# Performance work log

Hardware: AMD Instinct MI355X
Metric: run time of the kernel (lower is better)

The kernel has to match this reference:

```python
import jax, jax.numpy as jnp
import numpy as np

IN_F, OUT_F, GROUP = 4096, 4096, 128
N_GROUPS = IN_F // GROUP
NIB_SHIFTS = jnp.arange(8, dtype=jnp.int32) * 4  # 8 nibbles per int32


def dequantize(qweight, qzeros, scales, g_idx):
    """GPTQ/exllama 4-bit grouped dequant -> fp16 weight [K, N]."""
    # unpack qweight: [K//8, N] int32 -> [K//8, 8, N] nibbles -> [K, N]
    w_q = (qweight[:, None, :] >> NIB_SHIFTS[None, :, None]) & 0xF
    w_q = w_q.reshape(-1, qweight.shape[1])  # [K, N]
    # unpack qzeros: [G, N//8] int32 -> [G, N//8, 8] -> [G, N]
    z_q = (qzeros[:, :, None] >> NIB_SHIFTS[None, None, :]) & 0xF
    z_q = z_q.reshape(qzeros.shape[0], -1)  # [G, N]
    # exllama stores zero-points minus one: w = (q - (z + 1)) * scale
    z_rows = z_q[g_idx]            # [K, N] int32
    s_rows = scales[g_idx]         # [K, N] fp16
    return (w_q - z_rows - 1).astype(jnp.float16) * s_rows


def setup_inputs() -> dict:
    key = jax.random.key(0)
    k_x, k_qw, k_qz, k_s, k_b = jax.random.split(key, 5)
    x = jax.random.normal(k_x, (4, 2048, IN_F), dtype=jnp.float16)
    qweight = jax.random.randint(k_qw, (IN_F // 8, OUT_F), 0, 2147483647, dtype=jnp.int32)
    qzeros = jax.random.randint(k_qz, (N_GROUPS, OUT_F // 8), 0, 2147483647, dtype=jnp.int32)
    scales = (jax.random.uniform(k_s, (N_GROUPS, OUT_F), dtype=jnp.float32) * 0.01 + 0.001).astype(jnp.float16)
    g_idx = (jnp.arange(IN_F, dtype=jnp.int32) // GROUP).astype(jnp.int32)
    bias = (jax.random.normal(k_b, (OUT_F,), dtype=jnp.float32) * 0.02).astype(jnp.float16)
    return {"x": x, "qweight": qweight, "qzeros": qzeros, "scales": scales, "g_idx": g_idx, "bias": bias}


def reference(x, qweight, qzeros, scales, g_idx, bias):
    W = dequantize(qweight, qzeros, scales, g_idx)      # [K, N] fp16
    lead = x.shape[:-1]
    out = jnp.dot(x.reshape(-1, x.shape[-1]), W)        # fp16 GEMM, [T, N]
    out = out + bias
    return out.reshape(lead + (W.shape[1],))
```

## Files before the change

### kernel.cpp

```cpp
#include <hip/hip_runtime.h>
#include <hip/hip_bf16.h>
#include <stdint.h>

#define M_TOT 8192
#define N_TOT 4096
#define K_TOT 4096
#define GROUP 128


using f32x4  = __attribute__((ext_vector_type(4))) float;
using bf16x8 = __attribute__((ext_vector_type(8))) __bf16;

typedef __attribute__((address_space(3))) void as3_void;
typedef const __attribute__((address_space(1))) void as1_void;

__global__ __launch_bounds__(256) void cast_x(const float* __restrict__ x,
                                              __bf16* __restrict__ xb) {
    const size_t t = (size_t)blockIdx.x * 256 + threadIdx.x;
    const float4 f0 = *(const float4*)(x + t * 8);
    const float4 f1 = *(const float4*)(x + t * 8 + 4);
    bf16x8 v;
    v[0]=(__bf16)f0.x; v[1]=(__bf16)f0.y; v[2]=(__bf16)f0.z; v[3]=(__bf16)f0.w;
    v[4]=(__bf16)f1.x; v[5]=(__bf16)f1.y; v[6]=(__bf16)f1.z; v[7]=(__bf16)f1.w;
    *(bf16x8*)(xb + t * 8) = v;
}

__global__ __launch_bounds__(256) void dequant_w(
    const int*   __restrict__ qweight,
    const int*   __restrict__ qzeros,
    const float* __restrict__ scales,
    const int*   __restrict__ g_idx,
    __bf16* __restrict__ Wt)
{
    __shared__ __align__(16) unsigned short T[64 * 72];
    const int k0  = blockIdx.x * 64;
    const int n0  = blockIdx.y * 64;
    const int g   = g_idx[k0];
    const int tid = threadIdx.x;

    #pragma unroll
    for (int i = 0; i < 2; ++i) {
        const int idx = tid + i * 256;
        const int r   = idx >> 6;
        const int n   = idx & 63;
        const int qi  = qweight[(size_t)((k0 >> 3) + r) * N_TOT + n0 + n];
        const int zi  = qzeros[g * (N_TOT / 8) + ((n0 + n) >> 3)];
        const float s = scales[g * N_TOT + n0 + n];
        const float zs = (float)(((zi >> ((n & 7) * 4)) & 0xF) + 1) * s;
        bf16x8 v;
        #pragma unroll
        for (int j = 0; j < 8; ++j)
            v[j] = (__bf16)((float)((qi >> (4 * j)) & 0xF) * s - zs);
        *(bf16x8*)&T[n * 72 + r * 8] = v;
    }
    __syncthreads();

    const int n = tid >> 2;
    const int c = (tid & 3) * 16;
    const bf16x8 a = *(const bf16x8*)&T[n * 72 + c];
    const bf16x8 b = *(const bf16x8*)&T[n * 72 + c + 8];
    __bf16* dst = Wt + (size_t)(n0 + n) * K_TOT + k0 + c;
    *(bf16x8*)dst = a;
    *(bf16x8*)(dst + 8) = b;
}

#define GBM 256
#define GBN 256
#define GBK 64
#define NKT (K_TOT / GBK)

#define BAR() do { asm volatile("" ::: "memory"); \
                   __builtin_amdgcn_s_barrier();  \
                   asm volatile("" ::: "memory"); } while (0)
#define WAIT_LGKM0() asm volatile("s_waitcnt lgkmcnt(0)" ::: "memory")
#define WAIT_VM4()   asm volatile("s_waitcnt vmcnt(4)"   ::: "memory")
#define WAIT_VM0()   asm volatile("s_waitcnt vmcnt(0)"   ::: "memory")

#define GPHASE(q, STAGE_STMT)                                                 \
    {                                                                         \
        bf16x8 av[2][2];                                                      \
        _Pragma("unroll")                                                     \
        for (int ks = 0; ks < 2; ++ks) {                                      \
            av[0][ks] = ldA(buf, 2 * (q), ks);                                \
            av[1][ks] = ldA(buf, 2 * (q) + 1, ks);                            \
        }                                                                     \
        STAGE_STMT;                                                           \
        BAR();                                                                \
        WAIT_LGKM0();                                                         \
        __builtin_amdgcn_s_setprio(1);                                        \
        _Pragma("unroll")                                                     \
        for (int ks = 0; ks < 2; ++ks)                                        \
            _Pragma("unroll")                                                 \
            for (int mtl = 0; mtl < 2; ++mtl)                                 \
                _Pragma("unroll")                                             \
                for (int nt = 0; nt < 4; ++nt)                                \
                    acc[2 * (q) + mtl][nt] =                                  \
                        __builtin_amdgcn_mfma_f32_16x16x32_bf16(              \
                            av[mtl][ks], bv[nt][ks], acc[2 * (q) + mtl][nt],  \
                            0, 0, 0);                                         \
        __builtin_amdgcn_s_setprio(0);                                        \
        BAR();                                                                \
    }

__global__ __launch_bounds__(512, 2) void gemm8p(
    const __bf16* __restrict__ xb,
    const __bf16* __restrict__ Wt,
    const float*  __restrict__ bias,
    float* __restrict__ out)
{
    __shared__ __align__(16) unsigned short LDS[2][2][GBM * GBK];

    const int tid  = threadIdx.x;
    const int wid  = tid >> 6;
    const int lane = tid & 63;
    const int l15  = lane & 15;
    const int quad = lane >> 4;

    int bid = blockIdx.x;
    bid = (bid & 7) * (512 >> 3) + (bid >> 3);
    const int tn = bid & (N_TOT / GBN - 1);
    const int tm = bid >> 4;
    const int m0 = tm * GBM;
    const int n0 = tn * GBN;

    const int wm = (wid >> 2) * 128;
    const int wn = (wid & 3) * 64;

    f32x4 acc[8][4];
    #pragma unroll
    for (int i = 0; i < 8; ++i)
        #pragma unroll
        for (int j = 0; j < 4; ++j)
            acc[i][j] = (f32x4)0.f;

    auto stage = [&](int bf, int mat, int h, const __bf16* __restrict__ base,
                     int row0, int kt) {
        #pragma unroll
        for (int j = 0; j < 2; ++j) {
            const int c  = j * 512 + tid;
            const int rl = c >> 3;
            const int kc = (c & 7) ^ (rl & 7);
            const __bf16* ga = base + (size_t)(row0 + h * 128 + rl) * K_TOT
                             + kt * GBK + kc * 8;
            __builtin_amdgcn_global_load_lds((as1_void*)ga,
                (as3_void*)&LDS[bf][mat][h * 8192 + (j * 512 + wid * 64) * 8],
                16, 0, 0);
        }
    };
    auto ldA = [&](int bf, int mt, int ks) -> bf16x8 {
        const int r = wm + mt * 16 + l15;
        return *(const bf16x8*)
            &LDS[bf][0][r * GBK + (((ks * 4 + quad) ^ (r & 7)) << 3)];
    };
    auto ldB = [&](int bf, int nt, int ks) -> bf16x8 {
        const int r = wn + nt * 16 + l15;
        return *(const bf16x8*)
            &LDS[bf][1][r * GBK + (((ks * 4 + quad) ^ (r & 7)) << 3)];
    };

    stage(0, 0, 0, xb, m0, 0); stage(0, 0, 1, xb, m0, 0);
    stage(0, 1, 0, Wt, n0, 0); stage(0, 1, 1, Wt, n0, 0);
    stage(1, 1, 0, Wt, n0, 1); stage(1, 1, 1, Wt, n0, 1);
    WAIT_VM4();
    BAR();

    bf16x8 bv[4][2];

    for (int t = 0; t < NKT; ++t) {
        const int buf = t & 1;

        {
            #pragma unroll
            for (int nt = 0; nt < 4; ++nt)
                #pragma unroll
                for (int ks = 0; ks < 2; ++ks)
                    bv[nt][ks] = ldB(buf, nt, ks);
            bf16x8 av[2][2];
            #pragma unroll
            for (int ks = 0; ks < 2; ++ks) {
                av[0][ks] = ldA(buf, 0, ks);
                av[1][ks] = ldA(buf, 1, ks);
            }
            if (t + 1 < NKT) stage(buf ^ 1, 0, 0, xb, m0, t + 1);
            BAR();
            WAIT_LGKM0();
            __builtin_amdgcn_s_setprio(1);
            #pragma unroll
            for (int ks = 0; ks < 2; ++ks)
                #pragma unroll
                for (int mtl = 0; mtl < 2; ++mtl)
                    #pragma unroll
                    for (int nt = 0; nt < 4; ++nt)
                        acc[mtl][nt] = __builtin_amdgcn_mfma_f32_16x16x32_bf16(
                            av[mtl][ks], bv[nt][ks], acc[mtl][nt], 0, 0, 0);
            __builtin_amdgcn_s_setprio(0);
            BAR();
        }
        GPHASE(1, if (t + 1 < NKT) stage(buf ^ 1, 0, 1, xb, m0, t + 1));
        GPHASE(2, if (t + 2 < NKT) stage(buf, 1, 0, Wt, n0, t + 2));
        GPHASE(3, if (t + 2 < NKT) stage(buf, 1, 1, Wt, n0, t + 2));

        if (t < NKT - 2) { WAIT_VM4(); } else { WAIT_VM0(); }
    }

    #pragma unroll
    for (int nt = 0; nt < 4; ++nt) {
        const int col = n0 + wn + nt * 16 + l15;
        const float bb = bias[col];
        #pragma unroll
        for (int mt = 0; mt < 8; ++mt) {
            const int rowb = m0 + wm + mt * 16 + quad * 4;
            #pragma unroll
            for (int i = 0; i < 4; ++i)
                out[(size_t)(rowb + i) * N_TOT + col] = acc[mt][nt][i] + bb;
        }
    }
}

#define FBM 256
#define FBN 128
#define FBKP 72

__global__ __launch_bounds__(256, 2) void gptq_gemm_fused(
    const float* __restrict__ x, const int* __restrict__ qweight,
    const int* __restrict__ qzeros, const float* __restrict__ scales,
    const int* __restrict__ g_idx, const float* __restrict__ bias,
    float* __restrict__ out)
{
    __shared__ __align__(16) unsigned short As[FBM * FBKP];
    __shared__ __align__(16) unsigned short Bt[FBN * FBKP];

    const int tid  = threadIdx.x;
    const int wave = tid >> 6;
    const int lane = tid & 63;
    const int n0 = blockIdx.x * FBN;
    const int m0 = blockIdx.y * FBM;
    const int wm = (wave >> 1) * 64;
    const int wn = (wave & 1) * 64;
    const int l15  = lane & 15;
    const int quad = lane >> 4;

    f32x4 acc[2][4][4];
    #pragma unroll
    for (int mi = 0; mi < 2; ++mi)
        #pragma unroll
        for (int i = 0; i < 4; ++i)
            #pragma unroll
            for (int j = 0; j < 4; ++j)
                acc[mi][i][j] = (f32x4)0.f;

    const int nb  = tid & 31;
    const int r   = tid >> 5;
    const int zsh = (nb & 7) * 4;

    for (int kt = 0; kt < K_TOT / 64; ++kt) {
        const int k0 = kt * 64;
        #pragma unroll
        for (int i = 0; i < 8; ++i) {
            const int c   = tid + i * 256;
            const int row = c >> 3;
            const int cb  = (c & 7) << 3;
            const float* xp = x + (size_t)(m0 + row) * K_TOT + (k0 + cb);
            const float4 f0 = *(const float4*)xp;
            const float4 f1 = *(const float4*)(xp + 4);
            bf16x8 v;
            v[0]=(__bf16)f0.x; v[1]=(__bf16)f0.y; v[2]=(__bf16)f0.z; v[3]=(__bf16)f0.w;
            v[4]=(__bf16)f1.x; v[5]=(__bf16)f1.y; v[6]=(__bf16)f1.z; v[7]=(__bf16)f1.w;
            *(bf16x8*)&As[row * FBKP + cb] = v;
        }
        const int g    = g_idx[k0];
        const int qrow = (k0 >> 3) + r;
        #pragma unroll
        for (int dn = 0; dn < 4; ++dn) {
            const int n  = nb + dn * 32;
            const int qi = qweight[(size_t)qrow * N_TOT + (n0 + n)];
            const int zi = qzeros[g * (N_TOT / 8) + ((n0 + n) >> 3)];
            const float s = scales[g * N_TOT + (n0 + n)];
            const float zs = (float)(((zi >> zsh) & 0xF) + 1) * s;
            bf16x8 v;
            #pragma unroll
            for (int j = 0; j < 8; ++j)
                v[j] = (__bf16)((float)((qi >> (4 * j)) & 0xF) * s - zs);
            *(bf16x8*)&Bt[n * FBKP + r * 8] = v;
        }
        __syncthreads();
        #pragma unroll
        for (int ks = 0; ks < 2; ++ks) {
            bf16x8 bvv[4];
            #pragma unroll
            for (int nt = 0; nt < 4; ++nt)
                bvv[nt] = *(const bf16x8*)&Bt[(wn + nt * 16 + l15) * FBKP + ks * 32 + quad * 8];
            #pragma unroll
            for (int mi = 0; mi < 2; ++mi) {
                bf16x8 av[4];
                #pragma unroll
                for (int mt = 0; mt < 4; ++mt)
                    av[mt] = *(const bf16x8*)&As[(mi * 128 + wm + mt * 16 + l15) * FBKP + ks * 32 + quad * 8];
                #pragma unroll
                for (int mt = 0; mt < 4; ++mt)
                    #pragma unroll
                    for (int nt = 0; nt < 4; ++nt)
                        acc[mi][mt][nt] = __builtin_amdgcn_mfma_f32_16x16x32_bf16(
                            av[mt], bvv[nt], acc[mi][mt][nt], 0, 0, 0);
            }
        }
        __syncthreads();
    }
    #pragma unroll
    for (int mi = 0; mi < 2; ++mi)
        #pragma unroll
        for (int nt = 0; nt < 4; ++nt) {
            const int col = n0 + wn + nt * 16 + l15;
            const float bvv = bias[col];
            #pragma unroll
            for (int mt = 0; mt < 4; ++mt) {
                const int rowb = m0 + mi * 128 + wm + mt * 16 + quad * 4;
                #pragma unroll
                for (int i = 0; i < 4; ++i)
                    out[(size_t)(rowb + i) * N_TOT + col] = acc[mi][mt][nt][i] + bvv;
            }
        }
}

extern "C" void kernel_launch(void* const* d_in, const int* in_sizes, int n_in,
                              void* d_out, int out_size, void* d_ws, size_t ws_size,
                              hipStream_t stream) {
    const float* x  = (const float*)d_in[0];
    const int*   qw = (const int*)d_in[1];
    const int*   qz = (const int*)d_in[2];
    const float* sc = (const float*)d_in[3];
    const int*   gi = (const int*)d_in[4];
    const float* bs = (const float*)d_in[5];
    float* out = (float*)d_out;

    const size_t xb_bytes = (size_t)M_TOT * K_TOT * 2;
    const size_t wt_bytes = (size_t)N_TOT * K_TOT * 2;

    if (ws_size >= xb_bytes + wt_bytes) {
        __bf16* xb = (__bf16*)d_ws;
        __bf16* Wt = (__bf16*)((char*)d_ws + xb_bytes);
        cast_x<<<dim3((M_TOT * K_TOT) / (256 * 8)), dim3(256), 0, stream>>>(x, xb);
        dequant_w<<<dim3(K_TOT / 64, N_TOT / 64), dim3(256), 0, stream>>>(qw, qz, sc, gi, Wt);
        gemm8p<<<dim3((M_TOT / GBM) * (N_TOT / GBN)), dim3(512), 0, stream>>>(xb, Wt, bs, out);
    } else {
        gptq_gemm_fused<<<dim3(N_TOT / FBN, M_TOT / FBM), dim3(256), 0, stream>>>(
            x, qw, qz, sc, gi, bs, out);
    }
}
```

Before: 456.2 us.

## Triple-buffer A tiles in GEMM and merge cast and dequant kernels

The GEMM's A (activation) tiles move to a three-slot LDS ring, so they are prefetched two K-steps ahead like B. The vmcnt wait is raised to allow eight outstanding loads and now sits inside the last phase before its barrier. This is meant to hide global load latency for A better, at the cost of LDS use rising to 160KB, which leaves room for only one workgroup per CU. Separately, the x cast and the weight dequant are merged into a single prep launch to remove one kernel launch and let both parts run at the same time.

```diff
diff --git a/kernel.cpp b/kernel.cpp
--- a/kernel.cpp
+++ b/kernel.cpp
@@ -14,54 +14,55 @@
 typedef __attribute__((address_space(3))) void as3_void;
 typedef const __attribute__((address_space(1))) void as1_void;
 
-__global__ __launch_bounds__(256) void cast_x(const float* __restrict__ x,
-                                              __bf16* __restrict__ xb) {
-    const size_t t = (size_t)blockIdx.x * 256 + threadIdx.x;
-    const float4 f0 = *(const float4*)(x + t * 8);
-    const float4 f1 = *(const float4*)(x + t * 8 + 4);
-    bf16x8 v;
-    v[0]=(__bf16)f0.x; v[1]=(__bf16)f0.y; v[2]=(__bf16)f0.z; v[3]=(__bf16)f0.w;
-    v[4]=(__bf16)f1.x; v[5]=(__bf16)f1.y; v[6]=(__bf16)f1.z; v[7]=(__bf16)f1.w;
-    *(bf16x8*)(xb + t * 8) = v;
-}
-
-__global__ __launch_bounds__(256) void dequant_w(
+__global__ __launch_bounds__(256) void prep(
+    const float* __restrict__ x,
     const int*   __restrict__ qweight,
     const int*   __restrict__ qzeros,
     const float* __restrict__ scales,
     const int*   __restrict__ g_idx,
+    __bf16* __restrict__ xb,
     __bf16* __restrict__ Wt)
 {
-    __shared__ __align__(16) unsigned short T[64 * 72];
-    const int k0  = blockIdx.x * 64;
-    const int n0  = blockIdx.y * 64;
-    const int g   = g_idx[k0];
     const int tid = threadIdx.x;
-
-    #pragma unroll
-    for (int i = 0; i < 2; ++i) {
-        const int idx = tid + i * 256;
-        const int r   = idx >> 6;
-        const int n   = idx & 63;
-        const int qi  = qweight[(size_t)((k0 >> 3) + r) * N_TOT + n0 + n];
-        const int zi  = qzeros[g * (N_TOT / 8) + ((n0 + n) >> 3)];
-        const float s = scales[g * N_TOT + n0 + n];
-        const float zs = (float)(((zi >> ((n & 7) * 4)) & 0xF) + 1) * s;
+    if (blockIdx.x < 4096) {
+        __shared__ __align__(16) unsigned short T[64 * 72];
+        const int k0 = (blockIdx.x & 63) * 64;
+        const int n0 = (blockIdx.x >> 6) * 64;
+        const int g  = g_idx[k0];
+
+        #pragma unroll
+        for (int i = 0; i < 2; ++i) {
+            const int idx = tid + i * 256;
+            const int r   = idx >> 6;
+            const int n   = idx & 63;
+            const int qi  = qweight[(size_t)((k0 >> 3) + r) * N_TOT + n0 + n];
+            const int zi  = qzeros[g * (N_TOT / 8) + ((n0 + n) >> 3)];
+            const float s = scales[g * N_TOT + n0 + n];
+            const float zs = (float)(((zi >> ((n & 7) * 4)) & 0xF) + 1) * s;
+            bf16x8 v;
+            #pragma unroll
+            for (int j = 0; j < 8; ++j)
+                v[j] = (__bf16)((float)((qi >> (4 * j)) & 0xF) * s - zs);
+            *(bf16x8*)&T[n * 72 + r * 8] = v;
+        }
+        __syncthreads();
+
+        const int n = tid >> 2;
+        const int c = (tid & 3) * 16;
+        const bf16x8 a = *(const bf16x8*)&T[n * 72 + c];
+        const bf16x8 b = *(const bf16x8*)&T[n * 72 + c + 8];
+        __bf16* dst = Wt + (size_t)(n0 + n) * K_TOT + k0 + c;
+        *(bf16x8*)dst = a;
+        *(bf16x8*)(dst + 8) = b;
+    } else {
+        const size_t t = (size_t)(blockIdx.x - 4096) * 256 + tid;
+        const float4 f0 = *(const float4*)(x + t * 8);
+        const float4 f1 = *(const float4*)(x + t * 8 + 4);
         bf16x8 v;
-        #pragma unroll
-        for (int j = 0; j < 8; ++j)
-            v[j] = (__bf16)((float)((qi >> (4 * j)) & 0xF) * s - zs);
-        *(bf16x8*)&T[n * 72 + r * 8] = v;
-    }
-    __syncthreads();
-
-    const int n = tid >> 2;
-    const int c = (tid & 3) * 16;
-    const bf16x8 a = *(const bf16x8*)&T[n * 72 + c];
-    const bf16x8 b = *(const bf16x8*)&T[n * 72 + c + 8];
-    __bf16* dst = Wt + (size_t)(n0 + n) * K_TOT + k0 + c;
-    *(bf16x8*)dst = a;
-    *(bf16x8*)(dst + 8) = b;
+        v[0]=(__bf16)f0.x; v[1]=(__bf16)f0.y; v[2]=(__bf16)f0.z; v[3]=(__bf16)f0.w;
+        v[4]=(__bf16)f1.x; v[5]=(__bf16)f1.y; v[6]=(__bf16)f1.z; v[7]=(__bf16)f1.w;
+        *(bf16x8*)(xb + t * 8) = v;
+    }
 }
 
 #define GBM 256
@@ -73,16 +74,16 @@
                    __builtin_amdgcn_s_barrier();  \
                    asm volatile("" ::: "memory"); } while (0)
 #define WAIT_LGKM0() asm volatile("s_waitcnt lgkmcnt(0)" ::: "memory")
-#define WAIT_VM4()   asm volatile("s_waitcnt vmcnt(4)"   ::: "memory")
+#define WAIT_VM8()   asm volatile("s_waitcnt vmcnt(8)"   ::: "memory")
 #define WAIT_VM0()   asm volatile("s_waitcnt vmcnt(0)"   ::: "memory")
 
-#define GPHASE(q, STAGE_STMT)                                                 \
+#define GPHASE(q, STAGE_STMT, TAIL_STMT)                                      \
     {                                                                         \
         bf16x8 av[2][2];                                                      \
         _Pragma("unroll")                                                     \
         for (int ks = 0; ks < 2; ++ks) {                                      \
-            av[0][ks] = ldA(buf, 2 * (q), ks);                                \
-            av[1][ks] = ldA(buf, 2 * (q) + 1, ks);                            \
+            av[0][ks] = ldfrag(&Abuf[qa][0], wm, 2 * (q), ks);                \
+            av[1][ks] = ldfrag(&Abuf[qa][0], wm, 2 * (q) + 1, ks);            \
         }                                                                     \
         STAGE_STMT;                                                           \
         BAR();                                                                \
@@ -99,6 +100,7 @@
                             av[mtl][ks], bv[nt][ks], acc[2 * (q) + mtl][nt],  \
                             0, 0, 0);                                         \
         __builtin_amdgcn_s_setprio(0);                                        \
+        TAIL_STMT;                                                            \
         BAR();                                                                \
     }
 
@@ -108,7 +110,8 @@
     const float*  __restrict__ bias,
     float* __restrict__ out)
 {
-    __shared__ __align__(16) unsigned short LDS[2][2][GBM * GBK];
+    __shared__ __align__(16) unsigned short Abuf[3][GBM * GBK];
+    __shared__ __align__(16) unsigned short Bbuf[2][GBM * GBK];
 
     const int tid  = threadIdx.x;
     const int wid  = tid >> 6;
@@ -133,8 +136,8 @@
         for (int j = 0; j < 4; ++j)
             acc[i][j] = (f32x4)0.f;
 
-    auto stage = [&](int bf, int mat, int h, const __bf16* __restrict__ base,
-                     int row0, int kt) {
+    auto stage = [&](unsigned short* ldsb, int h,
+                     const __bf16* __restrict__ base, int row0, int kt) {
         #pragma unroll
         for (int j = 0; j < 2; ++j) {
             const int c  = j * 512 + tid;
@@ -143,45 +146,44 @@
             const __bf16* ga = base + (size_t)(row0 + h * 128 + rl) * K_TOT
                              + kt * GBK + kc * 8;
             __builtin_amdgcn_global_load_lds((as1_void*)ga,
-                (as3_void*)&LDS[bf][mat][h * 8192 + (j * 512 + wid * 64) * 8],
+                (as3_void*)&ldsb[h * 8192 + (j * 512 + wid * 64) * 8],
                 16, 0, 0);
         }
     };
-    auto ldA = [&](int bf, int mt, int ks) -> bf16x8 {
-        const int r = wm + mt * 16 + l15;
+    auto ldfrag = [&](const unsigned short* ldsb, int wbase, int mt,
+                      int ks) -> bf16x8 {
+        const int r = wbase + mt * 16 + l15;
         return *(const bf16x8*)
-            &LDS[bf][0][r * GBK + (((ks * 4 + quad) ^ (r & 7)) << 3)];
+            &ldsb[r * GBK + (((ks * 4 + quad) ^ (r & 7)) << 3)];
     };
-    auto ldB = [&](int bf, int nt, int ks) -> bf16x8 {
-        const int r = wn + nt * 16 + l15;
-        return *(const bf16x8*)
-            &LDS[bf][1][r * GBK + (((ks * 4 + quad) ^ (r & 7)) << 3)];
-    };
-
-    stage(0, 0, 0, xb, m0, 0); stage(0, 0, 1, xb, m0, 0);
-    stage(0, 1, 0, Wt, n0, 0); stage(0, 1, 1, Wt, n0, 0);
-    stage(1, 1, 0, Wt, n0, 1); stage(1, 1, 1, Wt, n0, 1);
-    WAIT_VM4();
+
+    stage(&Abuf[0][0], 0, xb, m0, 0); stage(&Abuf[0][0], 1, xb, m0, 0);
+    stage(&Bbuf[0][0], 0, Wt, n0, 0); stage(&Bbuf[0][0], 1, Wt, n0, 0);
+    stage(&Abuf[1][0], 0, xb, m0, 1); stage(&Abuf[1][0], 1, xb, m0, 1);
+    stage(&Bbuf[1][0], 0, Wt, n0, 1); stage(&Bbuf[1][0], 1, Wt, n0, 1);
+    WAIT_VM8();
     BAR();
 
     bf16x8 bv[4][2];
 
+    int qa = 0;
+    int qs = 2;
+    int p  = 0;
+
     for (int t = 0; t < NKT; ++t) {
-        const int buf = t & 1;
-
         {
             #pragma unroll
             for (int nt = 0; nt < 4; ++nt)
                 #pragma unroll
                 for (int ks = 0; ks < 2; ++ks)
-                    bv[nt][ks] = ldB(buf, nt, ks);
+                    bv[nt][ks] = ldfrag(&Bbuf[p][0], wn, nt, ks);
             bf16x8 av[2][2];
             #pragma unroll
             for (int ks = 0; ks < 2; ++ks) {
-                av[0][ks] = ldA(buf, 0, ks);
-                av[1][ks] = ldA(buf, 1, ks);
+                av[0][ks] = ldfrag(&Abuf[qa][0], wm, 0, ks);
+                av[1][ks] = ldfrag(&Abuf[qa][0], wm, 1, ks);
             }
-            if (t + 1 < NKT) stage(buf ^ 1, 0, 0, xb, m0, t + 1);
+            if (t + 2 < NKT) stage(&Abuf[qs][0], 0, xb, m0, t + 2);
             BAR();
             WAIT_LGKM0();
             __builtin_amdgcn_s_setprio(1);
@@ -196,11 +198,14 @@
             __builtin_amdgcn_s_setprio(0);
             BAR();
         }
-        GPHASE(1, if (t + 1 < NKT) stage(buf ^ 1, 0, 1, xb, m0, t + 1));
-        GPHASE(2, if (t + 2 < NKT) stage(buf, 1, 0, Wt, n0, t + 2));
-        GPHASE(3, if (t + 2 < NKT) stage(buf, 1, 1, Wt, n0, t + 2));
-
-        if (t < NKT - 2) { WAIT_VM4(); } else { WAIT_VM0(); }
+        GPHASE(1, if (t + 2 < NKT) stage(&Abuf[qs][0], 1, xb, m0, t + 2), );
+        GPHASE(2, if (t + 2 < NKT) stage(&Bbuf[p][0], 0, Wt, n0, t + 2), );
+        GPHASE(3, if (t + 2 < NKT) stage(&Bbuf[p][0], 1, Wt, n0, t + 2),
+               if (t < NKT - 2) { WAIT_VM8(); } else { WAIT_VM0(); });
+
+        qa = (qa == 2) ? 0 : qa + 1;
+        qs = (qs == 2) ? 0 : qs + 1;
+        p ^= 1;
     }
 
     #pragma unroll
@@ -339,9 +344,11 @@
     if (ws_size >= xb_bytes + wt_bytes) {
         __bf16* xb = (__bf16*)d_ws;
         __bf16* Wt = (__bf16*)((char*)d_ws + xb_bytes);
-        cast_x<<<dim3((M_TOT * K_TOT) / (256 * 8)), dim3(256), 0, stream>>>(x, xb);
-        dequant_w<<<dim3(K_TOT / 64, N_TOT / 64), dim3(256), 0, stream>>>(qw, qz, sc, gi, Wt);
-        gemm8p<<<dim3((M_TOT / GBM) * (N_TOT / GBN)), dim3(512), 0, stream>>>(xb, Wt, bs, out);
+        const int cast_blocks = (M_TOT * K_TOT) / (256 * 8);
+        prep<<<dim3(4096 + cast_blocks), dim3(256), 0, stream>>>(
+            x, qw, qz, sc, gi, xb, Wt);
+        gemm8p<<<dim3((M_TOT / GBM) * (N_TOT / GBN)), dim3(512), 0, stream>>>(
+            xb, Wt, bs, out);
     } else {
         gptq_gemm_fused<<<dim3(N_TOT / FBN, M_TOT / FBM), dim3(256), 0, stream>>>(
             x, qw, qz, sc, gi, bs, out);
```

Result: slower. 490.4 us (+7.5%).
